# Optimization experiments

Measured on AMD Instinct MI355X. Metric: run time of the kernel, lower is better.

## Reference

```python
import jax, jax.numpy as jnp
import numpy as np

DIM = 1024
NUM_HEADS = 16
HEAD_DIM = DIM // NUM_HEADS
SCALE = HEAD_DIM ** -0.5


def setup_inputs() -> dict:
    key = jax.random.key(0)
    k1, k2, k3, k4, k5, k6 = jax.random.split(key, 6)
    B, S, L = 4, 8192, 512
    x = jax.random.normal(k1, (B, S, DIM), dtype=jnp.float32)
    latents = jax.random.normal(k2, (B, L, DIM), dtype=jnp.float32)
    # Linear weights stored torch-style as (out_features, in_features)
    w_q = jax.random.normal(k3, (DIM, DIM), dtype=jnp.float32) * (DIM ** -0.5)
    w_kv = jax.random.normal(k4, (2 * DIM, DIM), dtype=jnp.float32) * (DIM ** -0.5)
    w_out = jax.random.normal(k5, (DIM, DIM), dtype=jnp.float32) * (DIM ** -0.5)
    b_out = jax.random.normal(k6, (DIM,), dtype=jnp.float32) * 0.01
    return {"x": x, "latents": latents, "w_q": w_q, "w_kv": w_kv,
            "w_out": w_out, "b_out": b_out}


def reference(x, latents, w_q, w_kv, w_out, b_out):
    B, L, _ = latents.shape
    S = x.shape[1]
    q = latents @ w_q.T                      # (B, L, dim)
    kv = x @ w_kv.T                          # (B, S, 2*dim)
    k, v = jnp.split(kv, 2, axis=-1)         # each (B, S, dim)
    q = q.reshape(B, L, NUM_HEADS, HEAD_DIM)
    k = k.reshape(B, S, NUM_HEADS, HEAD_DIM)
    v = v.reshape(B, S, NUM_HEADS, HEAD_DIM)
    # attention scores: (B, H, L, S)
    attn = jnp.einsum('blhd,bshd->bhls', q, k) * SCALE
    attn = jax.nn.softmax(attn, axis=-1)
    out = jnp.einsum('bhls,bshd->blhd', attn, v)  # (B, L, H, D)
    out = out.reshape(B, L, DIM)
    return out @ w_out.T + b_out
```

## Files before the change

### kernel.cpp

```cpp
#include <hip/hip_runtime.h>
#include <hip/hip_bf16.h>
#include <cstdint>
#include <cstddef>

#define B_ 4
#define S_ 8192
#define L_ 512
#define DIM 1024
#define NUM_HEADS 16
#define HEAD_DIM 64
#define SCHUNK 4096
#define NSEG 2
#define SEGKEYS (SCHUNK / NSEG)
#define SCALE 0.125f
#define L2E 1.44269504088896f
#define F_SC (SCALE * L2E)

typedef __bf16 bf16;
typedef __bf16 bf16x8 __attribute__((ext_vector_type(8)));
typedef float f32x4 __attribute__((ext_vector_type(4)));

#define AS1 __attribute__((address_space(1)))
#define AS3 __attribute__((address_space(3)))
#define GLDS(g, l) __builtin_amdgcn_global_load_lds((const AS1 void*)(g), (AS3 void*)(l), 16, 0, 0)
#define LGKM_FENCE() asm volatile("s_waitcnt lgkmcnt(0)" ::: "memory")
#define VMCNT4() asm volatile("s_waitcnt vmcnt(4)" ::: "memory")
#define VMCNT0() asm volatile("s_waitcnt vmcnt(0)" ::: "memory")
#define MFMA16(a, b, c) __builtin_amdgcn_mfma_f32_16x16x32_bf16((a), (b), (c), 0, 0, 0)

__global__ void detect_dtype(const unsigned int* __restrict__ x, int* __restrict__ flag) {
  int lane = threadIdx.x;
  int cnt = 0;
  for (int i = 0; i < 4; ++i) {
    unsigned int w = x[lane * 4 + i];
    unsigned int e = (w >> 7) & 0xFFu;
    cnt += (e >= 117u && e <= 129u) ? 1 : 0;
  }
  cnt += __shfl_xor(cnt, 1);
  cnt += __shfl_xor(cnt, 2);
  cnt += __shfl_xor(cnt, 4);
  cnt += __shfl_xor(cnt, 8);
  cnt += __shfl_xor(cnt, 16);
  cnt += __shfl_xor(cnt, 32);
  if (lane == 0) *flag = (cnt < 128) ? 1 : 0;
}

template<int REMAP>
__global__ __launch_bounds__(256) void conv_bf16(
    const void* __restrict__ in, bf16* __restrict__ out, int nchunk, int srow0,
    const int* __restrict__ flagp)
{
  const bool f32in = (*flagp != 0);
  for (int c = blockIdx.x * 256 + threadIdx.x; c < nchunk; c += gridDim.x * 256) {
    size_t gc;
    if (REMAP) {
      int r = c >> 7, cc = c & 127;
      gc = ((size_t)((r >> 12) * 8192 + srow0 + (r & 4095)) << 7) + cc;
    } else {
      gc = (size_t)c;
    }
    if (f32in) {
      const f32x4* g = (const f32x4*)in + gc * 2;
      f32x4 lo = g[0], hi = g[1];
      bf16x8 w;
      w[0] = (bf16)lo[0]; w[1] = (bf16)lo[1]; w[2] = (bf16)lo[2]; w[3] = (bf16)lo[3];
      w[4] = (bf16)hi[0]; w[5] = (bf16)hi[1]; w[6] = (bf16)hi[2]; w[7] = (bf16)hi[3];
      *(bf16x8*)(out + (size_t)c * 8) = w;
    } else {
      *(bf16x8*)(out + (size_t)c * 8) = ((const bf16x8*)in)[gc];
    }
  }
}

template<int HAS_BIAS, int DUAL_OUT, int NBN>
__global__ __launch_bounds__(256) void gemm_nt(
    const bf16* __restrict__ Ap, const bf16* __restrict__ Bwp,
    void* __restrict__ Cp, const void* __restrict__ biasp,
    int M, int N, int K, const int* __restrict__ flagp)
{
  __shared__ __align__(16) bf16 lA[128 * 64];
  __shared__ __align__(16) bf16 lB[128 * 64];
  const int tid = threadIdx.x;
  const int lane = tid & 63, quad = lane >> 4, l16 = lane & 15, wave = tid >> 6;
  const int wm = wave >> 1, wn = wave & 1;
  const int f = blockIdx.x;
  const int xcd = f & 7, sidx = f >> 3;
  const int bn = sidx % NBN;
  const int bm = xcd * (M >> 10) + sidx / NBN;
  const bool f32in = (HAS_BIAS || DUAL_OUT) ? (*flagp != 0) : false;

  f32x4 acc[4][4] = {};
  const int nK = K >> 6;
  for (int kb = 0; kb < nK; ++kb) {
    __syncthreads();
#pragma unroll
    for (int i = 0; i < 4; ++i) {
      int e = i * 256 + tid;
      int row = e >> 3, cp = e & 7, gcp = cp ^ (row & 7);
      const bf16* ga = Ap + (size_t)(bm * 128 + row) * K + kb * 64 + gcp * 8;
      GLDS(ga, lA + e * 8);
      const bf16* gb = Bwp + (size_t)(bn * 128 + row) * K + kb * 64 + gcp * 8;
      GLDS(gb, lB + e * 8);
    }
    __syncthreads();

#pragma unroll
    for (int ks = 0; ks < 2; ++ks) {
      bf16x8 af[4], bfr[4];
#pragma unroll
      for (int t = 0; t < 4; ++t) {
        int rowA = wm * 64 + t * 16 + l16;
        int ca = (ks * 4 + quad) ^ (rowA & 7);
        af[t] = *(const bf16x8*)(lA + rowA * 64 + ca * 8);
        int rowB = wn * 64 + t * 16 + l16;
        int cb = (ks * 4 + quad) ^ (rowB & 7);
        bfr[t] = *(const bf16x8*)(lB + rowB * 64 + cb * 8);
      }
#pragma unroll
      for (int tm = 0; tm < 4; ++tm)
#pragma unroll
        for (int tn = 0; tn < 4; ++tn)
          acc[tm][tn] = MFMA16(af[tm], bfr[tn], acc[tm][tn]);
    }
  }

#pragma unroll
  for (int tn = 0; tn < 4; ++tn) {
    int col = bn * 128 + wn * 64 + tn * 16 + l16;
    float bv = 0.0f;
    if (HAS_BIAS)
      bv = f32in ? ((const float*)biasp)[col] : (float)((const bf16*)biasp)[col];
#pragma unroll
    for (int tm = 0; tm < 4; ++tm) {
#pragma unroll
      for (int r = 0; r < 4; ++r) {
        int rowc = bm * 128 + wm * 64 + tm * 16 + quad * 4 + r;
        float v = acc[tm][tn][r] + bv;
        if (DUAL_OUT && f32in) {
          ((float*)Cp)[(size_t)rowc * N + col] = v;
        } else {
          ((bf16*)Cp)[(size_t)rowc * N + col] = (bf16)v;
        }
      }
    }
  }
}

__global__ __launch_bounds__(512) void gemm_kv_256(
    const bf16* __restrict__ Ap, const bf16* __restrict__ Bwp,
    bf16* __restrict__ Cp, bf16* __restrict__ C2p, int M, int K)
{
  __shared__ __align__(16) bf16 lA[2][256 * 64];
  __shared__ __align__(16) bf16 lB[2][256 * 64];
  const int tid = threadIdx.x;
  const int lane = tid & 63, quad = lane >> 4, l16 = lane & 15, wave = tid >> 6;
  const int wm = wave >> 2, wn = wave & 3;
  const int f = blockIdx.x;
  const int xcd = f & 7, sidx = f >> 3;
  const int bn = sidx & 7;
  const int bm = xcd * ((M >> 8) >> 3) + (sidx >> 3);
  const int nK = K >> 6;

#define STAGE_A(buf, half, kb) do {                                          \
  _Pragma("unroll")                                                          \
  for (int j = 0; j < 2; ++j) {                                              \
    int e = j * 512 + tid;                                                   \
    int row = e >> 3, cp = e & 7, gcp = cp ^ (row & 7);                      \
    const bf16* g = Ap + (size_t)(bm * 256 + (half) * 128 + row) * K         \
                       + (kb) * 64 + gcp * 8;                                \
    GLDS(g, &lA[buf][((half) * 128 + row) * 64 + cp * 8]);                   \
  } } while (0)
#define STAGE_B(buf, half, kb) do {                                          \
  _Pragma("unroll")                                                          \
  for (int j = 0; j < 2; ++j) {                                              \
    int e = j * 512 + tid;                                                   \
    int row = e >> 3, cp = e & 7, gcp = cp ^ (row & 7);                      \
    const bf16* g = Bwp + (size_t)(bn * 256 + (half) * 128 + row) * K        \
                        + (kb) * 64 + gcp * 8;                               \
    GLDS(g, &lB[buf][((half) * 128 + row) * 64 + cp * 8]);                   \
  } } while (0)

  f32x4 acc[8][4] = {};

  STAGE_A(0, 0, 0); STAGE_A(0, 1, 0); STAGE_B(0, 0, 0); STAGE_B(0, 1, 0);
  if (nK > 1) { STAGE_B(1, 0, 1); STAGE_B(1, 1, 1); VMCNT4(); }
  else VMCNT0();
  __builtin_amdgcn_s_barrier();

  for (int t = 0; t < nK; ++t) {
    const int cur = t & 1;
    bf16x8 breg[4][2];
#pragma unroll
    for (int p = 0; p < 4; ++p) {
      bf16x8 af[2][2];
      if (p == 0) {
#pragma unroll
        for (int nf = 0; nf < 4; ++nf)
#pragma unroll
          for (int ks = 0; ks < 2; ++ks) {
            int rowB = wn * 64 + nf * 16 + l16;
            int cb = (ks * 4 + quad) ^ (rowB & 7);
            breg[nf][ks] = *(const bf16x8*)&lB[cur][rowB * 64 + cb * 8];
          }
      }
#pragma unroll
      for (int mf2 = 0; mf2 < 2; ++mf2)
#pragma unroll
        for (int ks = 0; ks < 2; ++ks) {
          int rowA = wm * 128 + (p * 2 + mf2) * 16 + l16;
          int ca = (ks * 4 + quad) ^ (rowA & 7);
          af[mf2][ks] = *(const bf16x8*)&lA[cur][rowA * 64 + ca * 8];
        }
      LGKM_FENCE();

      if (p == 0) { if (t + 1 < nK) STAGE_A(cur ^ 1, 0, t + 1); }
      else if (p == 1) { if (t + 1 < nK) STAGE_A(cur ^ 1, 1, t + 1); }
      else if (p == 2) { if (t + 2 < nK) STAGE_B(cur, 0, t + 2); }
      else             { if (t + 2 < nK) STAGE_B(cur, 1, t + 2); }

      __builtin_amdgcn_s_barrier();

      __builtin_amdgcn_s_setprio(1);
#pragma unroll
      for (int mf2 = 0; mf2 < 2; ++mf2)
#pragma unroll
        for (int nf = 0; nf < 4; ++nf)
#pragma unroll
          for (int ks = 0; ks < 2; ++ks)
            acc[p * 2 + mf2][nf] = MFMA16(af[mf2][ks], breg[nf][ks], acc[p * 2 + mf2][nf]);
      __builtin_amdgcn_s_setprio(0);
    }
    if (t + 1 < nK) {
      if (t + 2 < nK) VMCNT4(); else VMCNT0();
      __builtin_amdgcn_s_barrier();
    }
  }

#pragma unroll
  for (int tn = 0; tn < 4; ++tn) {
    int col = bn * 256 + wn * 64 + tn * 16 + l16;
    bf16* outp = (col < 1024) ? Cp : C2p;
    int ocol = col & 1023;
#pragma unroll
    for (int tm = 0; tm < 8; ++tm)
#pragma unroll
      for (int r = 0; r < 4; ++r) {
        int rowc = bm * 256 + wm * 128 + tm * 16 + quad * 4 + r;
        outp[(size_t)rowc * 1024 + ocol] = (bf16)acc[tm][tn][r];
      }
  }
#undef STAGE_A
#undef STAGE_B
}

template<int FIRST>
__global__ __launch_bounds__(512) void attn_pass(
    const bf16* __restrict__ qb, const bf16* __restrict__ kc, const bf16* __restrict__ vc,
    float* __restrict__ Ost, float* __restrict__ lst)
{
  __shared__ __align__(16) bf16 lK[128 * 64];
  __shared__ __align__(16) bf16 lV[64][136];
  __shared__ __align__(16) bf16 pbuf[8][16][136];
  const int tid = threadIdx.x;
  const int lane = tid & 63, quad = lane >> 4, l16 = lane & 15, wave = tid >> 6;
  const int f = blockIdx.x;
  const int xcd = f & 7, sidx = f >> 3;
  const int lt = sidx & 3, ghi = sidx >> 2;
  const int g = ghi * 8 + xcd;
  const int h = g & 15, bs = g >> 4;
  const int b = bs >> 1, seg = bs & 1;
  const int l0 = lt * 128 + wave * 16;

  const bf16* qbase = qb + (size_t)(b * L_ + l0 + l16) * DIM + h * HEAD_DIM + quad * 8;
  bf16x8 qf0 = *(const bf16x8*)qbase;
  bf16x8 qf1 = *(const bf16x8*)(qbase + 32);

  f32x4 acc[4] = {};
  float lsum[4] = {0.0f, 0.0f, 0.0f, 0.0f};

  const int sbeg = seg * SEGKEYS;
  for (int s0 = sbeg; s0 < sbeg + SEGKEYS; s0 += 128) {
    __syncthreads();
#pragma unroll
    for (int i = 0; i < 2; ++i) {
      int e = i * 512 + tid;
      int row = e >> 3, cp = e & 7, gcp = cp ^ (row & 7);
      const bf16* gk = kc + (size_t)(b * SCHUNK + s0 + row) * DIM + h * HEAD_DIM + gcp * 8;
      GLDS(gk, lK + e * 8);
    }
#pragma unroll
    for (int i = 0; i < 2; ++i) {
      int e = i * 512 + tid;
      int row = e >> 3, cc = e & 7;
      bf16x8 vv = *(const bf16x8*)(vc + (size_t)(b * SCHUNK + s0 + row) * DIM + h * HEAD_DIM + cc * 8);
      int pg = (row >> 3) ^ cc;
#pragma unroll
      for (int j = 0; j < 8; ++j)
        lV[cc * 8 + j][pg * 8 + (row & 7)] = vv[j];
    }
    __syncthreads();

#pragma unroll
    for (int kt = 0; kt < 8; ++kt) {
      int rk = kt * 16 + l16;
      int p0c = quad ^ (rk & 7);
      int p1c = (4 + quad) ^ (rk & 7);
      bf16x8 kf0 = *(const bf16x8*)(lK + rk * 64 + p0c * 8);
      bf16x8 kf1 = *(const bf16x8*)(lK + rk * 64 + p1c * 8);
      f32x4 s4 = {};
      s4 = MFMA16(qf0, kf0, s4);
      s4 = MFMA16(qf1, kf1, s4);
#pragma unroll
      for (int r = 0; r < 4; ++r) {
        float a = exp2f(fminf(s4[r] * F_SC, 40.0f));
        lsum[r] += a;
        pbuf[wave][quad * 4 + r][kt * 16 + l16] = (bf16)a;
      }
    }
    LGKM_FENCE();
#pragma unroll
    for (int half = 0; half < 4; ++half) {
      bf16x8 pf = *(const bf16x8*)&pbuf[wave][l16][half * 32 + quad * 8];
#pragma unroll
      for (int t4 = 0; t4 < 4; ++t4) {
        int c = t4 * 16 + l16;
        int pg = (half * 4 + quad) ^ (c >> 3);
        bf16x8 vf = *(const bf16x8*)&lV[c][pg * 8];
        acc[t4] = MFMA16(pf, vf, acc[t4]);
      }
    }
  }

#pragma unroll
  for (int r = 0; r < 4; ++r) {
    lsum[r] += __shfl_xor(lsum[r], 1, 16);
    lsum[r] += __shfl_xor(lsum[r], 2, 16);
    lsum[r] += __shfl_xor(lsum[r], 4, 16);
    lsum[r] += __shfl_xor(lsum[r], 8, 16);
  }

  float* Oseg = Ost + (size_t)seg * (B_ * L_ * DIM);
  float* lseg = lst + (size_t)seg * (B_ * NUM_HEADS * L_);
#pragma unroll
  for (int r = 0; r < 4; ++r) {
    int l = l0 + quad * 4 + r;
    if (l16 == 0) {
      int si = (b * NUM_HEADS + h) * L_ + l;
      if (FIRST) lseg[si] = lsum[r];
      else       lseg[si] += lsum[r];
    }
  }
#pragma unroll
  for (int t4 = 0; t4 < 4; ++t4)
#pragma unroll
    for (int r = 0; r < 4; ++r) {
      int l = l0 + quad * 4 + r;
      size_t oi = (size_t)(b * L_ + l) * DIM + h * HEAD_DIM + t4 * 16 + l16;
      if (FIRST) Oseg[oi] = acc[t4][r];
      else       Oseg[oi] += acc[t4][r];
    }
}

__global__ __launch_bounds__(256) void combine_kernel(
    const float* __restrict__ Ost, const float* __restrict__ lst, bf16* __restrict__ ao)
{
  int idx = (blockIdx.x * 256 + threadIdx.x) * 4;
  int d0 = idx & (DIM - 1);
  int row = idx >> 10;
  int b = row >> 9, l = row & (L_ - 1);
  int h = d0 >> 6;
  int si = (b * NUM_HEADS + h) * L_ + l;
  float lv = lst[si] + lst[B_ * NUM_HEADS * L_ + si];
  float linv = 1.0f / lv;
  f32x4 o0 = *(const f32x4*)(Ost + idx);
  f32x4 o1 = *(const f32x4*)(Ost + (size_t)(B_ * L_ * DIM) + idx);
#pragma unroll
  for (int j = 0; j < 4; ++j)
    ao[idx + j] = (bf16)((o0[j] + o1[j]) * linv);
}

extern "C" void kernel_launch(void* const* d_in, const int* in_sizes, int n_in,
                              void* d_out, int out_size, void* d_ws, size_t ws_size,
                              hipStream_t stream)
{
  (void)in_sizes; (void)n_in; (void)out_size; (void)ws_size;
  const void* x       = d_in[0];
  const void* latents = d_in[1];
  const void* w_q     = d_in[2];
  const void* w_kv    = d_in[3];
  const void* w_out   = d_in[4];
  const void* b_out   = d_in[5];

  char* ws = (char*)d_ws;
  int*   flag  = (int*)ws;
  bf16*  qb    = (bf16*)(ws + ((size_t)1   << 20));
  float* lst   = (float*)(ws + ((size_t)5  << 20));
  bf16*  ao    = (bf16*)(ws + ((size_t)6   << 20));
  float* Ost   = (float*)(ws + ((size_t)10 << 20));
  bf16*  kc    = (bf16*)(ws + ((size_t)26 << 20));
  bf16*  latb  = (bf16*)(ws + ((size_t)26 << 20));
  bf16*  wqb   = (bf16*)(ws + ((size_t)30 << 20));
  bf16*  vc    = (bf16*)(ws + ((size_t)58 << 20));
  bf16*  xcb   = (bf16*)(ws + ((size_t)90 << 20));
  bf16*  wkvb  = (bf16*)(ws + ((size_t)122 << 20));
  bf16*  woutb = (bf16*)(ws + ((size_t)122 << 20));

  detect_dtype<<<1, 64, 0, stream>>>((const unsigned int*)x, flag);

  const int Mx = B_ * SCHUNK;

  conv_bf16<0><<<1024, 256, 0, stream>>>(latents, latb, (B_ * L_ * DIM) / 8, 0, flag);
  conv_bf16<0><<<512,  256, 0, stream>>>(w_q, wqb, (DIM * DIM) / 8, 0, flag);
  conv_bf16<0><<<1024, 256, 0, stream>>>(w_kv, wkvb, (2 * DIM * DIM) / 8, 0, flag);

  gemm_nt<0, 0, 8><<<128, 256, 0, stream>>>(
      latb, wqb, qb, nullptr, B_ * L_, DIM, DIM, flag);

  conv_bf16<1><<<2048, 256, 0, stream>>>(x, xcb, (Mx * DIM) / 8, 0, flag);
  gemm_kv_256<<<512, 512, 0, stream>>>(xcb, wkvb, kc, vc, Mx, DIM);
  attn_pass<1><<<512, 512, 0, stream>>>(qb, kc, vc, Ost, lst);

  conv_bf16<1><<<2048, 256, 0, stream>>>(x, xcb, (Mx * DIM) / 8, SCHUNK, flag);
  gemm_kv_256<<<512, 512, 0, stream>>>(xcb, wkvb, kc, vc, Mx, DIM);
  attn_pass<0><<<512, 512, 0, stream>>>(qb, kc, vc, Ost, lst);

  conv_bf16<0><<<512, 256, 0, stream>>>(w_out, woutb, (DIM * DIM) / 8, 0, flag);
  combine_kernel<<<(B_ * L_ * DIM / 4) / 256, 256, 0, stream>>>(Ost, lst, ao);

  gemm_nt<1, 1, 8><<<128, 256, 0, stream>>>(
      ao, woutb, d_out, b_out, B_ * L_, DIM, DIM, flag);
}
```

Measured before the change: 568.4 us.

## Merge conversion kernels and overlap second-chunk x conversion with attention

Replaces the separate dtype-detect kernel with an inline per-thread check. Merges the four initial conversions into one launch. Moves the second-half x conversion into extra blocks of the first attention pass so it runs alongside the attention work, and folds the w_out conversion into the combine kernel. The aim is to cut launch count and serialized memory-bound conversion time, at the cost of redundant detection reads in every thread and extra blocks competing with attention blocks for resources.

```diff
diff --git a/kernel.cpp b/kernel.cpp
--- a/kernel.cpp
+++ b/kernel.cpp
@@ -16,6 +16,11 @@
 #define L2E 1.44269504088896f
 #define F_SC (SCALE * L2E)
 
+#define XCH (B_ * SCHUNK * DIM / 8)
+#define LATCH (B_ * L_ * DIM / 8)
+#define WQCH (DIM * DIM / 8)
+#define WKVCH (2 * DIM * DIM / 8)
+
 typedef __bf16 bf16;
 typedef __bf16 bf16x8 __attribute__((ext_vector_type(8)));
 typedef float f32x4 __attribute__((ext_vector_type(4)));
@@ -28,46 +33,53 @@
 #define VMCNT0() asm volatile("s_waitcnt vmcnt(0)" ::: "memory")
 #define MFMA16(a, b, c) __builtin_amdgcn_mfma_f32_16x16x32_bf16((a), (b), (c), 0, 0, 0)
 
-__global__ void detect_dtype(const unsigned int* __restrict__ x, int* __restrict__ flag) {
-  int lane = threadIdx.x;
+__device__ __forceinline__ bool detect_f32(const void* xp) {
+  const unsigned int* x = (const unsigned int*)xp;
   int cnt = 0;
-  for (int i = 0; i < 4; ++i) {
-    unsigned int w = x[lane * 4 + i];
-    unsigned int e = (w >> 7) & 0xFFu;
+#pragma unroll
+  for (int i = 0; i < 32; ++i) {
+    unsigned int e = (x[i] >> 7) & 0xFFu;
     cnt += (e >= 117u && e <= 129u) ? 1 : 0;
   }
-  cnt += __shfl_xor(cnt, 1);
-  cnt += __shfl_xor(cnt, 2);
-  cnt += __shfl_xor(cnt, 4);
-  cnt += __shfl_xor(cnt, 8);
-  cnt += __shfl_xor(cnt, 16);
-  cnt += __shfl_xor(cnt, 32);
-  if (lane == 0) *flag = (cnt < 128) ? 1 : 0;
-}
-
-template<int REMAP>
-__global__ __launch_bounds__(256) void conv_bf16(
-    const void* __restrict__ in, bf16* __restrict__ out, int nchunk, int srow0,
-    const int* __restrict__ flagp)
-{
-  const bool f32in = (*flagp != 0);
-  for (int c = blockIdx.x * 256 + threadIdx.x; c < nchunk; c += gridDim.x * 256) {
-    size_t gc;
-    if (REMAP) {
+  return cnt < 16;
+}
+
+__device__ __forceinline__ void conv_chunk(
+    const void* in, bf16* out, size_t gc, size_t oc, bool f32in) {
+  if (f32in) {
+    const f32x4* g = (const f32x4*)in + gc * 2;
+    f32x4 lo = g[0], hi = g[1];
+    bf16x8 w;
+    w[0] = (bf16)lo[0]; w[1] = (bf16)lo[1]; w[2] = (bf16)lo[2]; w[3] = (bf16)lo[3];
+    w[4] = (bf16)hi[0]; w[5] = (bf16)hi[1]; w[6] = (bf16)hi[2]; w[7] = (bf16)hi[3];
+    *(bf16x8*)(out + oc * 8) = w;
+  } else {
+    *(bf16x8*)(out + oc * 8) = ((const bf16x8*)in)[gc];
+  }
+}
+
+__global__ __launch_bounds__(256) void conv_all(
+    const void* __restrict__ x, const void* __restrict__ lat,
+    const void* __restrict__ wq, const void* __restrict__ wkv,
+    bf16* __restrict__ xcb, bf16* __restrict__ latb,
+    bf16* __restrict__ wqb, bf16* __restrict__ wkvb)
+{
+  const bool f32in = detect_f32(x);
+  const int TOT = XCH + LATCH + WQCH + WKVCH;
+  for (int c = blockIdx.x * 256 + threadIdx.x; c < TOT; c += gridDim.x * 256) {
+    if (c < XCH) {
       int r = c >> 7, cc = c & 127;
-      gc = ((size_t)((r >> 12) * 8192 + srow0 + (r & 4095)) << 7) + cc;
+      size_t gc = ((size_t)((r >> 12) * 8192 + (r & 4095)) << 7) + cc;
+      conv_chunk(x, xcb, gc, (size_t)c, f32in);
+    } else if (c < XCH + LATCH) {
+      int k = c - XCH;
+      conv_chunk(lat, latb, (size_t)k, (size_t)k, f32in);
+    } else if (c < XCH + LATCH + WQCH) {
+      int k = c - XCH - LATCH;
+      conv_chunk(wq, wqb, (size_t)k, (size_t)k, f32in);
     } else {
-      gc = (size_t)c;
-    }
-    if (f32in) {
-      const f32x4* g = (const f32x4*)in + gc * 2;
-      f32x4 lo = g[0], hi = g[1];
-      bf16x8 w;
-      w[0] = (bf16)lo[0]; w[1] = (bf16)lo[1]; w[2] = (bf16)lo[2]; w[3] = (bf16)lo[3];
-      w[4] = (bf16)hi[0]; w[5] = (bf16)hi[1]; w[6] = (bf16)hi[2]; w[7] = (bf16)hi[3];
-      *(bf16x8*)(out + (size_t)c * 8) = w;
-    } else {
-      *(bf16x8*)(out + (size_t)c * 8) = ((const bf16x8*)in)[gc];
+      int k = c - XCH - LATCH - WQCH;
+      conv_chunk(wkv, wkvb, (size_t)k, (size_t)k, f32in);
     }
   }
 }
@@ -76,7 +88,7 @@
 __global__ __launch_bounds__(256) void gemm_nt(
     const bf16* __restrict__ Ap, const bf16* __restrict__ Bwp,
     void* __restrict__ Cp, const void* __restrict__ biasp,
-    int M, int N, int K, const int* __restrict__ flagp)
+    int M, int N, int K, const void* __restrict__ xdet)
 {
   __shared__ __align__(16) bf16 lA[128 * 64];
   __shared__ __align__(16) bf16 lB[128 * 64];
@@ -87,7 +99,7 @@
   const int xcd = f & 7, sidx = f >> 3;
   const int bn = sidx % NBN;
   const int bm = xcd * (M >> 10) + sidx / NBN;
-  const bool f32in = (HAS_BIAS || DUAL_OUT) ? (*flagp != 0) : false;
+  const bool f32in = (HAS_BIAS || DUAL_OUT) ? detect_f32(xdet) : false;
 
   f32x4 acc[4][4] = {};
   const int nK = K >> 6;
@@ -256,11 +268,24 @@
 template<int FIRST>
 __global__ __launch_bounds__(512) void attn_pass(
     const bf16* __restrict__ qb, const bf16* __restrict__ kc, const bf16* __restrict__ vc,
-    float* __restrict__ Ost, float* __restrict__ lst)
+    float* __restrict__ Ost, float* __restrict__ lst,
+    const void* __restrict__ x, bf16* __restrict__ xcb, int srow0)
 {
   __shared__ __align__(16) bf16 lK[128 * 64];
   __shared__ __align__(16) bf16 lV[64][136];
   __shared__ __align__(16) bf16 pbuf[8][16][136];
+
+  if (blockIdx.x >= 512) {
+    const bool f32in = detect_f32(x);
+    const int nb = gridDim.x - 512;
+    for (int c = (blockIdx.x - 512) * 512 + threadIdx.x; c < XCH; c += nb * 512) {
+      int r = c >> 7, cc = c & 127;
+      size_t gc = ((size_t)((r >> 12) * 8192 + srow0 + (r & 4095)) << 7) + cc;
+      conv_chunk(x, xcb, gc, (size_t)c, f32in);
+    }
+    return;
+  }
+
   const int tid = threadIdx.x;
   const int lane = tid & 63, quad = lane >> 4, l16 = lane & 15, wave = tid >> 6;
   const int f = blockIdx.x;
@@ -361,9 +386,17 @@
     }
 }
 
-__global__ __launch_bounds__(256) void combine_kernel(
-    const float* __restrict__ Ost, const float* __restrict__ lst, bf16* __restrict__ ao)
-{
+__global__ __launch_bounds__(256) void combine_wout(
+    const float* __restrict__ Ost, const float* __restrict__ lst, bf16* __restrict__ ao,
+    const void* __restrict__ x, const void* __restrict__ wout, bf16* __restrict__ woutb)
+{
+  if (blockIdx.x >= 2048) {
+    const bool f32in = detect_f32(x);
+    const int nb = gridDim.x - 2048;
+    for (int c = (blockIdx.x - 2048) * 256 + threadIdx.x; c < WQCH; c += nb * 256)
+      conv_chunk(wout, woutb, (size_t)c, (size_t)c, f32in);
+    return;
+  }
   int idx = (blockIdx.x * 256 + threadIdx.x) * 4;
   int d0 = idx & (DIM - 1);
   int row = idx >> 10;
@@ -392,7 +425,6 @@
   const void* b_out   = d_in[5];
 
   char* ws = (char*)d_ws;
-  int*   flag  = (int*)ws;
   bf16*  qb    = (bf16*)(ws + ((size_t)1   << 20));
   float* lst   = (float*)(ws + ((size_t)5  << 20));
   bf16*  ao    = (bf16*)(ws + ((size_t)6   << 20));
@@ -405,28 +437,23 @@
   bf16*  wkvb  = (bf16*)(ws + ((size_t)122 << 20));
   bf16*  woutb = (bf16*)(ws + ((size_t)122 << 20));
 
-  detect_dtype<<<1, 64, 0, stream>>>((const unsigned int*)x, flag);
-
   const int Mx = B_ * SCHUNK;
 
-  conv_bf16<0><<<1024, 256, 0, stream>>>(latents, latb, (B_ * L_ * DIM) / 8, 0, flag);
-  conv_bf16<0><<<512,  256, 0, stream>>>(w_q, wqb, (DIM * DIM) / 8, 0, flag);
-  conv_bf16<0><<<1024, 256, 0, stream>>>(w_kv, wkvb, (2 * DIM * DIM) / 8, 0, flag);
+  conv_all<<<2048, 256, 0, stream>>>(x, latents, w_q, w_kv, xcb, latb, wqb, wkvb);
 
   gemm_nt<0, 0, 8><<<128, 256, 0, stream>>>(
-      latb, wqb, qb, nullptr, B_ * L_, DIM, DIM, flag);
-
-  conv_bf16<1><<<2048, 256, 0, stream>>>(x, xcb, (Mx * DIM) / 8, 0, flag);
+      latb, wqb, qb, nullptr, B_ * L_, DIM, DIM, x);
+
   gemm_kv_256<<<512, 512, 0, stream>>>(xcb, wkvb, kc, vc, Mx, DIM);
-  attn_pass<1><<<512, 512, 0, stream>>>(qb, kc, vc, Ost, lst);
-
-  conv_bf16<1><<<2048, 256, 0, stream>>>(x, xcb, (Mx * DIM) / 8, SCHUNK, flag);
+
+  attn_pass<1><<<1024, 512, 0, stream>>>(qb, kc, vc, Ost, lst, x, xcb, SCHUNK);
+
   gemm_kv_256<<<512, 512, 0, stream>>>(xcb, wkvb, kc, vc, Mx, DIM);
-  attn_pass<0><<<512, 512, 0, stream>>>(qb, kc, vc, Ost, lst);
-
-  conv_bf16<0><<<512, 256, 0, stream>>>(w_out, woutb, (DIM * DIM) / 8, 0, flag);
-  combine_kernel<<<(B_ * L_ * DIM / 4) / 256, 256, 0, stream>>>(Ost, lst, ao);
+
+  attn_pass<0><<<512, 512, 0, stream>>>(qb, kc, vc, Ost, lst, x, xcb, 0);
+
+  combine_wout<<<2560, 256, 0, stream>>>(Ost, lst, ao, x, w_out, woutb);
 
   gemm_nt<1, 1, 8><<<128, 256, 0, stream>>>(
-      ao, woutb, d_out, b_out, B_ * L_, DIM, DIM, flag);
-}
+      ao, woutb, d_out, b_out, B_ * L_, DIM, DIM, x);
+}
```

Result: faster. 557.2 us (-2.0%).
